# Performance work log

Measured on AMD Instinct MI355X. Metric: run time of the kernel, lower is better.

The kernel has to match this reference:

```python
import jax, jax.numpy as jnp
import numpy as np

EPS = 1e-5

def _act_quant(x):
    # per-token int8 absmax quantization with STE passthrough
    s = 127.0 / jnp.clip(jnp.max(jnp.abs(x), axis=-1, keepdims=True), EPS, None)
    xq = jnp.clip(jnp.round(x * s), -128.0, 127.0) / s
    return x + jax.lax.stop_gradient(xq - x)

def _weight_quant(w):
    # ternary {-1,0,1} abs-mean quantization with STE passthrough
    s = 1.0 / jnp.clip(jnp.mean(jnp.abs(w)), EPS, None)
    wq = jnp.clip(jnp.round(w * s), -1.0, 1.0) / s
    return w + jax.lax.stop_gradient(wq - w)

def bitlinear(x, w, b=None):
    y = _act_quant(x) @ _weight_quant(w).T
    return y if b is None else y + b

def setup_inputs() -> dict:
    key = jax.random.key(0)
    ks = jax.random.split(key, 6)
    B, T, C = 64, 256, 1024
    std = 1.0 / np.sqrt(C)
    return {
        "x": jax.random.normal(ks[0], (B, T, C), dtype=jnp.float32),
        "Wq": jax.random.normal(ks[1], (C, C), dtype=jnp.float32) * std,
        "Wk": jax.random.normal(ks[2], (C, C), dtype=jnp.float32) * std,
        "Wv": jax.random.normal(ks[3], (C, C), dtype=jnp.float32) * std,
        "Wp": jax.random.normal(ks[4], (C, C), dtype=jnp.float32) * std,
        "bp": jnp.zeros((C,), dtype=jnp.float32),
        "n_head": 16,
    }

def reference(x, Wq, Wk, Wv, Wp, bp, n_head):
    B, T, C = x.shape
    hd = C // n_head
    def heads(t):  # [B,T,C] -> [B,H,T,hd]
        return t.reshape(B, T, n_head, hd).transpose(0, 2, 1, 3)
    q = heads(bitlinear(x, Wq))
    k = heads(bitlinear(x, Wk))
    v = heads(bitlinear(x, Wv))
    attn = jnp.einsum("bhqd,bhkd->bhqk", q, k) * (1.0 / np.sqrt(hd))
    causal = jnp.tril(jnp.ones((T, T), dtype=bool))
    attn = jnp.where(causal, attn, -jnp.inf)
    attn = jax.nn.softmax(attn, axis=-1)
    y = jnp.einsum("bhqk,bhkd->bhqd", attn, v)
    y = y.transpose(0, 2, 1, 3).reshape(B, T, C)
    return bitlinear(y, Wp, bp)
```

## Files before the change

kernel.cpp:

```cpp
#include <hip/hip_runtime.h>
#include <math.h>

#define AS1 __attribute__((address_space(1)))
#define AS3 __attribute__((address_space(3)))

typedef unsigned short u16;
typedef signed char i8;
typedef short bf16x8 __attribute__((ext_vector_type(8)));
typedef float f32x4 __attribute__((ext_vector_type(4)));
typedef int i32x4 __attribute__((ext_vector_type(4)));

static constexpr int BB = 64, T = 256, C = 1024, H = 16, HD = 64;
static constexpr int M = BB * T;
static constexpr float EPSF = 1e-5f;

static constexpr size_t W8_OFF   = 0;
static constexpr size_t XQ8_OFF  = 4ull  << 20;
static constexpr size_t RSX_OFF  = 20ull << 20;
static constexpr size_t RSY_OFF  = (20ull << 20) + (64 << 10);
static constexpr size_t WSUM_OFF = (20ull << 20) + (128 << 10);
static constexpr size_t WPART_OFF= WSUM_OFF + 64;
static constexpr size_t QB_OFF   = 21ull << 20;
static constexpr size_t KB_OFF   = 53ull << 20;
static constexpr size_t VB_OFF   = 85ull << 20;

__device__ __forceinline__ u16 f2bf_rne(float f) {
    unsigned x = __float_as_uint(f);
    unsigned r = x + 0x7FFF + ((x >> 16) & 1);
    return (u16)(r >> 16);
}

__global__ __launch_bounds__(256) void wsum1_kernel(const float* __restrict__ Wq,
    const float* __restrict__ Wk, const float* __restrict__ Wv,
    const float* __restrict__ Wp, double* __restrict__ wpart)
{
    const int mat = blockIdx.x >> 6;
    const float* W = (mat == 0) ? Wq : (mat == 1) ? Wk : (mat == 2) ? Wv : Wp;
    const int t = threadIdx.x;
    const int base = (blockIdx.x & 63) * 256 + t;
    double s = 0.0;
    for (int i = 0; i < 64; ++i) s += (double)fabsf(W[base + (i << 14)]);
    #pragma unroll
    for (int off = 32; off >= 1; off >>= 1) s += __shfl_down(s, off);
    __shared__ double red[4];
    if ((t & 63) == 0) red[t >> 6] = s;
    __syncthreads();
    if (t == 0) wpart[blockIdx.x] = red[0] + red[1] + red[2] + red[3];
}

__global__ __launch_bounds__(256) void wsum2_kernel(const double* __restrict__ wpart,
                                                    double* __restrict__ wsum)
{
    const int t = threadIdx.x;
    double s = wpart[t];
    #pragma unroll
    for (int off = 32; off >= 1; off >>= 1) s += __shfl_down(s, off);
    if ((t & 63) == 0) wsum[t >> 6] = s;
}

__global__ __launch_bounds__(256) void wquant_kernel(const float* __restrict__ Wq,
    const float* __restrict__ Wk, const float* __restrict__ Wv,
    const float* __restrict__ Wp, const double* __restrict__ wsum,
    i8* __restrict__ w8)
{
    const int mat = blockIdx.x >> 10;
    const float* W = (mat == 0) ? Wq : (mat == 1) ? Wk : (mat == 2) ? Wv : Wp;
    const float mean = (float)(wsum[mat] * (1.0 / 1048576.0));
    const float s = 1.0f / fmaxf(mean, EPSF);
    const int idx = (blockIdx.x & 1023) * 256 + threadIdx.x;
    float4 w = ((const float4*)W)[idx];
    char4 o;
    o.x = (i8)(int)fminf(fmaxf(rintf(w.x * s), -1.f), 1.f);
    o.y = (i8)(int)fminf(fmaxf(rintf(w.y * s), -1.f), 1.f);
    o.z = (i8)(int)fminf(fmaxf(rintf(w.z * s), -1.f), 1.f);
    o.w = (i8)(int)fminf(fmaxf(rintf(w.w * s), -1.f), 1.f);
    ((char4*)(w8 + (size_t)mat * 1048576))[idx] = o;
}

__global__ __launch_bounds__(256) void actquant_kernel(const float* __restrict__ x,
    i8* __restrict__ xq, float* __restrict__ rs)
{
    const int row = blockIdx.x;
    const int t = threadIdx.x;
    float4 v = ((const float4*)(x + (size_t)row * C))[t];
    float m = fmaxf(fmaxf(fabsf(v.x), fabsf(v.y)), fmaxf(fabsf(v.z), fabsf(v.w)));
    #pragma unroll
    for (int off = 32; off >= 1; off >>= 1) m = fmaxf(m, __shfl_down(m, off));
    __shared__ float red[4];
    if ((t & 63) == 0) red[t >> 6] = m;
    __syncthreads();
    float mm = fmaxf(fmaxf(red[0], red[1]), fmaxf(red[2], red[3]));
    mm = fmaxf(mm, EPSF);
    const float s = 127.0f / mm;
    if (t == 0) rs[row] = mm / 127.0f;
    char4 o;
    o.x = (i8)(int)fminf(fmaxf(rintf(v.x * s), -128.f), 127.f);
    o.y = (i8)(int)fminf(fmaxf(rintf(v.y * s), -128.f), 127.f);
    o.z = (i8)(int)fminf(fmaxf(rintf(v.z * s), -128.f), 127.f);
    o.w = (i8)(int)fminf(fmaxf(rintf(v.w * s), -128.f), 127.f);
    ((char4*)(xq + (size_t)row * C))[t] = o;
}

template<bool QKV>
__global__ __launch_bounds__(256) void gemm_kernel(const i8* __restrict__ A,
    const i8* __restrict__ w8, const float* __restrict__ rs_row,
    const double* __restrict__ wsum, u16* __restrict__ qb, u16* __restrict__ kb,
    u16* __restrict__ vb, float* __restrict__ outp, const float* __restrict__ bias)
{
    constexpr int K = 1024, N = 1024;
    __shared__ __align__(16) i8 Asm[128 * 64];
    __shared__ __align__(16) i8 Bsm[128 * 64];

    const int t = threadIdx.x;
    const int m0 = blockIdx.y * 128;
    const int nb  = QKV ? (int)(blockIdx.x & 7) : (int)blockIdx.x;
    const int mat = QKV ? (int)(blockIdx.x >> 3) : 3;
    const int n0 = nb * 128;
    const i8* Bw = w8 + (size_t)mat * 1048576;

    const int lane = t & 63, wave = t >> 6;
    const int wm = wave >> 1, wn = wave & 1;
    const int mr = lane & 15, quad = lane >> 4;

    i32x4 acc[4][4];
    #pragma unroll
    for (int i = 0; i < 4; ++i)
        #pragma unroll
        for (int j = 0; j < 4; ++j) acc[i][j] = (i32x4){0, 0, 0, 0};

    const int c0 = t, c1 = t + 256;
    const int r0 = c0 >> 2, g0 = ((c0 & 3) ^ ((r0 >> 1) & 3)) * 16;
    const int r1 = c1 >> 2, g1 = ((c1 & 3) ^ ((r1 >> 1) & 3)) * 16;
    const i8* a0 = A  + (size_t)(m0 + r0) * K + g0;
    const i8* a1 = A  + (size_t)(m0 + r1) * K + g1;
    const i8* b0 = Bw + (size_t)(n0 + r0) * K + g0;
    const i8* b1 = Bw + (size_t)(n0 + r1) * K + g1;

    const int swq = (quad ^ ((mr >> 1) & 3)) * 16;

    for (int k0 = 0; k0 < K; k0 += 64) {
        __builtin_amdgcn_global_load_lds((const AS1 void*)(a0 + k0), (AS3 void*)&Asm[c0 * 16], 16, 0, 0);
        __builtin_amdgcn_global_load_lds((const AS1 void*)(a1 + k0), (AS3 void*)&Asm[c1 * 16], 16, 0, 0);
        __builtin_amdgcn_global_load_lds((const AS1 void*)(b0 + k0), (AS3 void*)&Bsm[c0 * 16], 16, 0, 0);
        __builtin_amdgcn_global_load_lds((const AS1 void*)(b1 + k0), (AS3 void*)&Bsm[c1 * 16], 16, 0, 0);
        __syncthreads();
        i32x4 af[4], bf[4];
        #pragma unroll
        for (int i = 0; i < 4; ++i)
            af[i] = *(const i32x4*)&Asm[(wm * 64 + i * 16 + mr) * 64 + swq];
        #pragma unroll
        for (int j = 0; j < 4; ++j)
            bf[j] = *(const i32x4*)&Bsm[(wn * 64 + j * 16 + mr) * 64 + swq];
        #pragma unroll
        for (int i = 0; i < 4; ++i)
            #pragma unroll
            for (int j = 0; j < 4; ++j)
                acc[i][j] = __builtin_amdgcn_mfma_i32_16x16x64_i8(af[i], bf[j], acc[i][j], 0, 0, 0);
        __syncthreads();
    }

    float wsc = fmaxf((float)(wsum[mat] * (1.0 / 1048576.0)), EPSF);
    if (QKV && mat == 0) wsc *= 0.125f;
    u16* ob = QKV ? ((mat == 0) ? qb : (mat == 1) ? kb : vb) : nullptr;

    #pragma unroll
    for (int i = 0; i < 4; ++i) {
        const int gr0 = m0 + wm * 64 + i * 16 + quad * 4;
        #pragma unroll
        for (int r = 0; r < 4; ++r) {
            const int grow = gr0 + r;
            const float sc = rs_row[grow] * wsc;
            #pragma unroll
            for (int j = 0; j < 4; ++j) {
                const int gcol = n0 + wn * 64 + j * 16 + mr;
                const float vv = (float)acc[i][j][r] * sc;
                if (QKV) {
                    ob[(size_t)grow * N + gcol] = f2bf_rne(vv);
                } else {
                    outp[(size_t)grow * N + gcol] = vv + bias[gcol];
                }
            }
        }
    }
}

__global__ __launch_bounds__(256) void attn_kernel(const u16* __restrict__ qb,
    const u16* __restrict__ kb, const u16* __restrict__ vb, float* __restrict__ y)
{
    __shared__ __align__(16) u16 Vsm[64 * 264];
    __shared__ __align__(16) u16 Psm[4][2][16 * 40];

    const int t = threadIdx.x;
    const int qt = 3 - (int)(blockIdx.x >> 10);
    const int bh = blockIdx.x & 1023;
    const int b = bh >> 4, h = bh & 15;
    const int w = t >> 6, lane = t & 63;
    const int cl = lane & 15, quad = lane >> 4;
    const size_t gb = (size_t)(b * T) * 1024 + h * 64;

    const int jn = (qt + 1) * 64;

    {
        const int j_in = t & 63;
        const int d0 = (t >> 6) * 16;
        for (int jg = 0; jg < jn; jg += 64) {
            const u16* vr = vb + gb + (size_t)(jg + j_in) * 1024 + d0;
            bf16x8 v0 = *(const bf16x8*)vr;
            bf16x8 v1 = *(const bf16x8*)(vr + 8);
            #pragma unroll
            for (int i = 0; i < 8; ++i) {
                Vsm[(d0 + i) * 264 + jg + j_in]     = (u16)v0[i];
                Vsm[(d0 + 8 + i) * 264 + jg + j_in] = (u16)v1[i];
            }
        }
    }
    __syncthreads();

    const int qrow = qt * 64 + w * 16;
    const int jtiles = (qrow >> 4) + 1;

    const u16* qrp = qb + gb + (size_t)(qrow + cl) * 1024 + quad * 8;
    bf16x8 qf0 = *(const bf16x8*)qrp;
    bf16x8 qf1 = *(const bf16x8*)(qrp + 32);

    f32x4 S[16];
    #pragma unroll
    for (int i = 0; i < 16; ++i) S[i] = (f32x4){0.f, 0.f, 0.f, 0.f};

    const u16* krp = kb + gb + (size_t)cl * 1024 + quad * 8;
    #pragma unroll
    for (int jt = 0; jt < 16; ++jt) {
        if (jt < jtiles) {
            const u16* kp = krp + (size_t)(jt * 16) * 1024;
            bf16x8 kf0 = *(const bf16x8*)kp;
            bf16x8 kf1 = *(const bf16x8*)(kp + 32);
            S[jt] = __builtin_amdgcn_mfma_f32_16x16x32_bf16(qf0, kf0, S[jt], 0, 0, 0);
            S[jt] = __builtin_amdgcn_mfma_f32_16x16x32_bf16(qf1, kf1, S[jt], 0, 0, 0);
            if (jt == jtiles - 1) {
                #pragma unroll
                for (int r = 0; r < 4; ++r)
                    if (cl > quad * 4 + r) S[jt][r] = -INFINITY;
            }
        }
    }

    float mrow[4], lrow[4];
    #pragma unroll
    for (int r = 0; r < 4; ++r) mrow[r] = -INFINITY;
    #pragma unroll
    for (int jt = 0; jt < 16; ++jt) if (jt < jtiles) {
        #pragma unroll
        for (int r = 0; r < 4; ++r) mrow[r] = fmaxf(mrow[r], S[jt][r]);
    }
    #pragma unroll
    for (int r = 0; r < 4; ++r) {
        #pragma unroll
        for (int off = 1; off < 16; off <<= 1)
            mrow[r] = fmaxf(mrow[r], __shfl_xor(mrow[r], off));
    }
    #pragma unroll
    for (int r = 0; r < 4; ++r) lrow[r] = 0.f;
    #pragma unroll
    for (int jt = 0; jt < 16; ++jt) if (jt < jtiles) {
        #pragma unroll
        for (int r = 0; r < 4; ++r) {
            float p = __expf(S[jt][r] - mrow[r]);
            S[jt][r] = p;
            lrow[r] += p;
        }
    }
    #pragma unroll
    for (int r = 0; r < 4; ++r) {
        #pragma unroll
        for (int off = 1; off < 16; off <<= 1)
            lrow[r] += __shfl_xor(lrow[r], off);
    }

    f32x4 O[4];
    #pragma unroll
    for (int i = 0; i < 4; ++i) O[i] = (f32x4){0.f, 0.f, 0.f, 0.f};

    #pragma unroll
    for (int jc = 0; jc < 8; ++jc) {
        if (jc * 2 < jtiles) {
            u16* Pw = &Psm[w][jc & 1][0];
            #pragma unroll
            for (int s2 = 0; s2 < 2; ++s2) {
                const int jt = jc * 2 + s2;
                #pragma unroll
                for (int r = 0; r < 4; ++r) {
                    u16 pv = 0;
                    if (jt < jtiles) pv = f2bf_rne(S[jt][r]);
                    Pw[(quad * 4 + r) * 40 + s2 * 16 + cl] = pv;
                }
            }
            __builtin_amdgcn_s_waitcnt(0xc07f);
            bf16x8 pf = *(const bf16x8*)&Pw[cl * 40 + quad * 8];
            #pragma unroll
            for (int dt = 0; dt < 4; ++dt) {
                bf16x8 vf = *(const bf16x8*)&Vsm[(dt * 16 + cl) * 264 + jc * 32 + quad * 8];
                O[dt] = __builtin_amdgcn_mfma_f32_16x16x32_bf16(pf, vf, O[dt], 0, 0, 0);
            }
        }
    }

    float inv[4];
    #pragma unroll
    for (int r = 0; r < 4; ++r) inv[r] = 1.0f / lrow[r];
    #pragma unroll
    for (int dt = 0; dt < 4; ++dt)
        #pragma unroll
        for (int r = 0; r < 4; ++r)
            y[gb + (size_t)(qrow + quad * 4 + r) * 1024 + dt * 16 + cl] = O[dt][r] * inv[r];
}

extern "C" void kernel_launch(void* const* d_in, const int* in_sizes, int n_in,
                              void* d_out, int out_size, void* d_ws, size_t ws_size,
                              hipStream_t stream) {
    (void)in_sizes; (void)n_in; (void)out_size; (void)ws_size;
    const float* x  = (const float*)d_in[0];
    const float* Wq = (const float*)d_in[1];
    const float* Wk = (const float*)d_in[2];
    const float* Wv = (const float*)d_in[3];
    const float* Wp = (const float*)d_in[4];
    const float* bp = (const float*)d_in[5];
    float* out = (float*)d_out;
    char* ws = (char*)d_ws;

    i8*     w8   = (i8*)(ws + W8_OFF);
    i8*     xq8  = (i8*)(ws + XQ8_OFF);
    float*  rsx  = (float*)(ws + RSX_OFF);
    float*  rsy  = (float*)(ws + RSY_OFF);
    double* wsum = (double*)(ws + WSUM_OFF);
    double* wpart= (double*)(ws + WPART_OFF);
    u16*    qb   = (u16*)(ws + QB_OFF);
    u16*    kb   = (u16*)(ws + KB_OFF);
    u16*    vb   = (u16*)(ws + VB_OFF);

    wsum1_kernel<<<256, 256, 0, stream>>>(Wq, Wk, Wv, Wp, wpart);
    wsum2_kernel<<<1, 256, 0, stream>>>(wpart, wsum);
    wquant_kernel<<<4096, 256, 0, stream>>>(Wq, Wk, Wv, Wp, wsum, w8);
    actquant_kernel<<<M, 256, 0, stream>>>(x, xq8, rsx);

    gemm_kernel<true ><<<dim3(24, 128), 256, 0, stream>>>(xq8, w8, rsx, wsum, qb, kb, vb, nullptr, nullptr);

    attn_kernel<<<4 * 1024, 256, 0, stream>>>(qb, kb, vb, out);

    actquant_kernel<<<M, 256, 0, stream>>>(out, xq8, rsy);
    gemm_kernel<false><<<dim3(8, 128), 256, 0, stream>>>(xq8, w8, rsy, wsum, nullptr, nullptr, nullptr, out, bp);
}
```

Before: 341.0 us.

## Write V transposed from GEMM epilogue and keep P in registers in attention

The QKV GEMM epilogue now writes V in a transposed [b, channel, t] layout with vectorized ushort4 stores. This lets the attention kernel read V fragments straight from global memory instead of staging a transposed copy in LDS behind a block barrier. The attention kernel also computes S transposed (K×Q), so each lane holds one query column. The softmax reductions then need only two cross-quad shuffles, and the P fragments for the PV MFMA are rebuilt with register shuffles instead of an LDS round trip. The cost is that the same V data is re-read from global/L2 by each of the four waves, and V stores in the GEMM epilogue become strided.

New measurement: 336.6 us. Within noise of the previous version (-1.3%).

```diff
diff --git a/kernel.cpp b/kernel.cpp
--- a/kernel.cpp
+++ b/kernel.cpp
@@ -22,7 +22,7 @@
 static constexpr size_t WPART_OFF= WSUM_OFF + 64;
 static constexpr size_t QB_OFF   = 21ull << 20;
 static constexpr size_t KB_OFF   = 53ull << 20;
-static constexpr size_t VB_OFF   = 85ull << 20;
+static constexpr size_t VT_OFF   = 85ull << 20;
 
 __device__ __forceinline__ u16 f2bf_rne(float f) {
     unsigned x = __float_as_uint(f);
@@ -105,7 +105,7 @@
 __global__ __launch_bounds__(256) void gemm_kernel(const i8* __restrict__ A,
     const i8* __restrict__ w8, const float* __restrict__ rs_row,
     const double* __restrict__ wsum, u16* __restrict__ qb, u16* __restrict__ kb,
-    u16* __restrict__ vb, float* __restrict__ outp, const float* __restrict__ bias)
+    u16* __restrict__ vt, float* __restrict__ outp, const float* __restrict__ bias)
 {
     constexpr int K = 1024, N = 1024;
     __shared__ __align__(16) i8 Asm[128 * 64];
@@ -161,8 +161,28 @@
 
     float wsc = fmaxf((float)(wsum[mat] * (1.0 / 1048576.0)), EPSF);
     if (QKV && mat == 0) wsc *= 0.125f;
-    u16* ob = QKV ? ((mat == 0) ? qb : (mat == 1) ? kb : vb) : nullptr;
-
+
+    if (QKV && mat == 2) {
+        #pragma unroll
+        for (int i = 0; i < 4; ++i) {
+            const int gr0 = m0 + wm * 64 + i * 16 + quad * 4;
+            const int bb = gr0 >> 8, tl = gr0 & 255;
+            const float4 rs4 = *(const float4*)(rs_row + gr0);
+            #pragma unroll
+            for (int j = 0; j < 4; ++j) {
+                const int gcol = n0 + wn * 64 + j * 16 + mr;
+                ushort4 o;
+                o.x = f2bf_rne((float)acc[i][j][0] * rs4.x * wsc);
+                o.y = f2bf_rne((float)acc[i][j][1] * rs4.y * wsc);
+                o.z = f2bf_rne((float)acc[i][j][2] * rs4.z * wsc);
+                o.w = f2bf_rne((float)acc[i][j][3] * rs4.w * wsc);
+                *(ushort4*)(vt + (size_t)(bb * 1024 + gcol) * 256 + tl) = o;
+            }
+        }
+        return;
+    }
+
+    u16* ob = QKV ? ((mat == 0) ? qb : kb) : nullptr;
     #pragma unroll
     for (int i = 0; i < 4; ++i) {
         const int gr0 = m0 + wm * 64 + i * 16 + quad * 4;
@@ -185,11 +205,8 @@
 }
 
 __global__ __launch_bounds__(256) void attn_kernel(const u16* __restrict__ qb,
-    const u16* __restrict__ kb, const u16* __restrict__ vb, float* __restrict__ y)
-{
-    __shared__ __align__(16) u16 Vsm[64 * 264];
-    __shared__ __align__(16) u16 Psm[4][2][16 * 40];
-
+    const u16* __restrict__ kb, const u16* __restrict__ vt, float* __restrict__ y)
+{
     const int t = threadIdx.x;
     const int qt = 3 - (int)(blockIdx.x >> 10);
     const int bh = blockIdx.x & 1023;
@@ -197,24 +214,7 @@
     const int w = t >> 6, lane = t & 63;
     const int cl = lane & 15, quad = lane >> 4;
     const size_t gb = (size_t)(b * T) * 1024 + h * 64;
-
-    const int jn = (qt + 1) * 64;
-
-    {
-        const int j_in = t & 63;
-        const int d0 = (t >> 6) * 16;
-        for (int jg = 0; jg < jn; jg += 64) {
-            const u16* vr = vb + gb + (size_t)(jg + j_in) * 1024 + d0;
-            bf16x8 v0 = *(const bf16x8*)vr;
-            bf16x8 v1 = *(const bf16x8*)(vr + 8);
-            #pragma unroll
-            for (int i = 0; i < 8; ++i) {
-                Vsm[(d0 + i) * 264 + jg + j_in]     = (u16)v0[i];
-                Vsm[(d0 + 8 + i) * 264 + jg + j_in] = (u16)v1[i];
-            }
-        }
-    }
-    __syncthreads();
+    const u16* vtb = vt + (size_t)(b * 1024 + h * 64) * 256;
 
     const int qrow = qt * 64 + w * 16;
     const int jtiles = (qrow >> 4) + 1;
@@ -223,9 +223,9 @@
     bf16x8 qf0 = *(const bf16x8*)qrp;
     bf16x8 qf1 = *(const bf16x8*)(qrp + 32);
 
-    f32x4 S[16];
-    #pragma unroll
-    for (int i = 0; i < 16; ++i) S[i] = (f32x4){0.f, 0.f, 0.f, 0.f};
+    f32x4 Sp[16];
+    #pragma unroll
+    for (int i = 0; i < 16; ++i) Sp[i] = (f32x4){0.f, 0.f, 0.f, 0.f};
 
     const u16* krp = kb + gb + (size_t)cl * 1024 + quad * 8;
     #pragma unroll
@@ -234,79 +234,74 @@
             const u16* kp = krp + (size_t)(jt * 16) * 1024;
             bf16x8 kf0 = *(const bf16x8*)kp;
             bf16x8 kf1 = *(const bf16x8*)(kp + 32);
-            S[jt] = __builtin_amdgcn_mfma_f32_16x16x32_bf16(qf0, kf0, S[jt], 0, 0, 0);
-            S[jt] = __builtin_amdgcn_mfma_f32_16x16x32_bf16(qf1, kf1, S[jt], 0, 0, 0);
+            Sp[jt] = __builtin_amdgcn_mfma_f32_16x16x32_bf16(kf0, qf0, Sp[jt], 0, 0, 0);
+            Sp[jt] = __builtin_amdgcn_mfma_f32_16x16x32_bf16(kf1, qf1, Sp[jt], 0, 0, 0);
             if (jt == jtiles - 1) {
                 #pragma unroll
                 for (int r = 0; r < 4; ++r)
-                    if (cl > quad * 4 + r) S[jt][r] = -INFINITY;
-            }
-        }
-    }
-
-    float mrow[4], lrow[4];
-    #pragma unroll
-    for (int r = 0; r < 4; ++r) mrow[r] = -INFINITY;
+                    if (quad * 4 + r > cl) Sp[jt][r] = -INFINITY;
+            }
+        }
+    }
+
+    float mx = -INFINITY;
     #pragma unroll
     for (int jt = 0; jt < 16; ++jt) if (jt < jtiles) {
         #pragma unroll
-        for (int r = 0; r < 4; ++r) mrow[r] = fmaxf(mrow[r], S[jt][r]);
-    }
-    #pragma unroll
-    for (int r = 0; r < 4; ++r) {
-        #pragma unroll
-        for (int off = 1; off < 16; off <<= 1)
-            mrow[r] = fmaxf(mrow[r], __shfl_xor(mrow[r], off));
-    }
-    #pragma unroll
-    for (int r = 0; r < 4; ++r) lrow[r] = 0.f;
+        for (int r = 0; r < 4; ++r) mx = fmaxf(mx, Sp[jt][r]);
+    }
+    mx = fmaxf(mx, __shfl_xor(mx, 16));
+    mx = fmaxf(mx, __shfl_xor(mx, 32));
+    float l = 0.f;
     #pragma unroll
     for (int jt = 0; jt < 16; ++jt) if (jt < jtiles) {
         #pragma unroll
         for (int r = 0; r < 4; ++r) {
-            float p = __expf(S[jt][r] - mrow[r]);
-            S[jt][r] = p;
-            lrow[r] += p;
-        }
-    }
-    #pragma unroll
-    for (int r = 0; r < 4; ++r) {
-        #pragma unroll
-        for (int off = 1; off < 16; off <<= 1)
-            lrow[r] += __shfl_xor(lrow[r], off);
-    }
+            float p = __expf(Sp[jt][r] - mx);
+            Sp[jt][r] = p;
+            l += p;
+        }
+    }
+    l += __shfl_xor(l, 16);
+    l += __shfl_xor(l, 32);
 
     f32x4 O[4];
     #pragma unroll
     for (int i = 0; i < 4; ++i) O[i] = (f32x4){0.f, 0.f, 0.f, 0.f};
 
+    const int s01 = ((quad & 1) << 5) + cl;
+    const bool lo = quad < 2;
     #pragma unroll
     for (int jc = 0; jc < 8; ++jc) {
         if (jc * 2 < jtiles) {
-            u16* Pw = &Psm[w][jc & 1][0];
-            #pragma unroll
-            for (int s2 = 0; s2 < 2; ++s2) {
-                const int jt = jc * 2 + s2;
-                #pragma unroll
-                for (int r = 0; r < 4; ++r) {
-                    u16 pv = 0;
-                    if (jt < jtiles) pv = f2bf_rne(S[jt][r]);
-                    Pw[(quad * 4 + r) * 40 + s2 * 16 + cl] = pv;
-                }
-            }
-            __builtin_amdgcn_s_waitcnt(0xc07f);
-            bf16x8 pf = *(const bf16x8*)&Pw[cl * 40 + quad * 8];
+            int pk[2][2];
+            #pragma unroll
+            for (int s = 0; s < 2; ++s) {
+                const f32x4 v = Sp[jc * 2 + s];
+                pk[s][0] = (int)((unsigned)f2bf_rne(v[0]) | ((unsigned)f2bf_rne(v[1]) << 16));
+                pk[s][1] = (int)((unsigned)f2bf_rne(v[2]) | ((unsigned)f2bf_rne(v[3]) << 16));
+            }
+            int a0 = __shfl(pk[0][0], s01),      a1 = __shfl(pk[0][1], s01);
+            int a2 = __shfl(pk[0][0], s01 + 16), a3 = __shfl(pk[0][1], s01 + 16);
+            int b0 = __shfl(pk[1][0], s01),      b1 = __shfl(pk[1][1], s01);
+            int b2 = __shfl(pk[1][0], s01 + 16), b3 = __shfl(pk[1][1], s01 + 16);
+            union { int i[4]; bf16x8 v; } af;
+            af.i[0] = lo ? a0 : b0;
+            af.i[1] = lo ? a1 : b1;
+            af.i[2] = lo ? a2 : b2;
+            af.i[3] = lo ? a3 : b3;
+            const u16* vp = vtb + (size_t)cl * 256 + jc * 32 + quad * 8;
             #pragma unroll
             for (int dt = 0; dt < 4; ++dt) {
-                bf16x8 vf = *(const bf16x8*)&Vsm[(dt * 16 + cl) * 264 + jc * 32 + quad * 8];
-                O[dt] = __builtin_amdgcn_mfma_f32_16x16x32_bf16(pf, vf, O[dt], 0, 0, 0);
+                bf16x8 vf = *(const bf16x8*)(vp + (size_t)dt * 16 * 256);
+                O[dt] = __builtin_amdgcn_mfma_f32_16x16x32_bf16(af.v, vf, O[dt], 0, 0, 0);
             }
         }
     }
 
     float inv[4];
     #pragma unroll
-    for (int r = 0; r < 4; ++r) inv[r] = 1.0f / lrow[r];
+    for (int r = 0; r < 4; ++r) inv[r] = 1.0f / __shfl(l, quad * 4 + r);
     #pragma unroll
     for (int dt = 0; dt < 4; ++dt)
         #pragma unroll
@@ -335,16 +330,16 @@
     double* wpart= (double*)(ws + WPART_OFF);
     u16*    qb   = (u16*)(ws + QB_OFF);
     u16*    kb   = (u16*)(ws + KB_OFF);
-    u16*    vb   = (u16*)(ws + VB_OFF);
+    u16*    vt   = (u16*)(ws + VT_OFF);
 
     wsum1_kernel<<<256, 256, 0, stream>>>(Wq, Wk, Wv, Wp, wpart);
     wsum2_kernel<<<1, 256, 0, stream>>>(wpart, wsum);
     wquant_kernel<<<4096, 256, 0, stream>>>(Wq, Wk, Wv, Wp, wsum, w8);
     actquant_kernel<<<M, 256, 0, stream>>>(x, xq8, rsx);
 
-    gemm_kernel<true ><<<dim3(24, 128), 256, 0, stream>>>(xq8, w8, rsx, wsum, qb, kb, vb, nullptr, nullptr);
-
-    attn_kernel<<<4 * 1024, 256, 0, stream>>>(qb, kb, vb, out);
+    gemm_kernel<true ><<<dim3(24, 128), 256, 0, stream>>>(xq8, w8, rsx, wsum, qb, kb, vt, nullptr, nullptr);
+
+    attn_kernel<<<4 * 1024, 256, 0, stream>>>(qb, kb, vt, out);
 
     actquant_kernel<<<M, 256, 0, stream>>>(out, xq8, rsy);
     gemm_kernel<false><<<dim3(8, 128), 256, 0, stream>>>(xq8, w8, rsy, wsum, nullptr, nullptr, nullptr, out, bp);
```
